# Kernel tuning notes

Measured on AMD Instinct MI355X. Metric: run time of the kernel, lower is better.

The kernel has to match this reference:

```python
import jax, jax.numpy as jnp
import numpy as np

DIM = 384
HEADS = 12
K = 3          # kernel_size
PAD = 1
STRIDE = 1
B, H, W = 8, 56, 56


def conv1x1(x, w, b=None):
    # x: [B,C,H,W], w: [O,C]
    y = jnp.einsum('bchw,oc->bohw', x, w)
    if b is not None:
        y = y + b[None, :, None, None]
    return y


def unfold(x, k, p, s):
    # torch nn.Unfold: returns patches [B, C, k*k, nH, nW], kernel row-major, channel-major overall
    Bx, C, Hx, Wx = x.shape
    nH = (Hx + 2 * p - k) // s + 1
    nW = (Wx + 2 * p - k) // s + 1
    xp = jnp.pad(x, ((0, 0), (0, 0), (p, p), (p, p)))
    cols = [xp[:, :, i:i + s * nH:s, j:j + s * nW:s] for i in range(k) for j in range(k)]
    return jnp.stack(cols, axis=2), nH, nW


def fold(col, Hx, Wx, k, p, s):
    # torch F.fold (col2im): scatter-add overlapping windows. col: [B, C, k*k, nH, nW]
    Bx, C, _, nH, nW = col.shape
    canvas = jnp.zeros((Bx, C, Hx + 2 * p, Wx + 2 * p), col.dtype)
    idx = 0
    for i in range(k):
        for j in range(k):
            canvas = canvas.at[:, :, i:i + s * nH:s, j:j + s * nW:s].add(col[:, :, idx])
            idx += 1
    return canvas[:, :, p:p + Hx, p:p + Wx]


def setup_inputs() -> dict:
    key = jax.random.key(0)
    ks = jax.random.split(key, 5)
    k2 = K * K
    x = jax.random.normal(ks[0], (B, DIM, H, W), dtype=jnp.float32)
    v_w = jax.random.normal(ks[1], (DIM, DIM), dtype=jnp.float32) * 0.02
    v_b = jnp.zeros((DIM,), dtype=jnp.float32)
    attn_w = jax.random.normal(ks[2], (k2 * k2 * HEADS, DIM), dtype=jnp.float32) * 0.02
    proj_w = jax.random.normal(ks[3], (DIM, DIM), dtype=jnp.float32) * 0.02
    return {'x': x, 'v_w': v_w, 'v_b': v_b, 'attn_w': attn_w, 'proj_w': proj_w}


def reference(x, v_w, v_b, attn_w, proj_w):
    Bx, C, Hx, Wx = x.shape
    k2 = K * K
    hd = C // HEADS  # head dim
    # value projection + unfold into overlapping k x k windows
    v = conv1x1(x, v_w, v_b)
    vcol, nH, nW = unfold(v, K, PAD, STRIDE)        # [B, C, k2, nH, nW]
    L = nH * nW
    v = vcol.reshape(Bx, HEADS, hd, k2, L)          # split C = (heads, hd), heads slow
    v = v.transpose(0, 1, 4, 3, 2)                  # [B, n, L, k2(d), hd]
    # adaptive avg pool to (nH, nW); with stride=1 this is identity (pool window 1)
    ph, pw = Hx // nH, Wx // nW
    xp = x.reshape(Bx, C, nH, ph, nW, pw).mean(axis=(3, 5))
    # per-pixel attention logits, channel layout = ((i*k2 + d)*HEADS + head)
    a = jnp.einsum('bchw,oc->bohw', xp, attn_w)     # [B, k2*k2*n, nH, nW]
    a = a.reshape(Bx, k2, k2, HEADS, L)             # [B, i, d, n, L]
    a = a.transpose(0, 3, 4, 1, 2)                  # [B, n, L, i, d]
    a = jax.nn.softmax(a, axis=-1)
    out = jnp.einsum('bnlid,bnldh->bnlih', a, v)    # [B, n, L, i, hd]
    out = out.transpose(0, 1, 4, 3, 2)              # [B, n, hd, i, L] -> channel (n*hd+h)
    out = out.reshape(Bx, C, k2, nH, nW)
    out = fold(out, Hx, Wx, K, PAD, STRIDE)         # scatter-add windows back
    return conv1x1(out, proj_w)
```

## Files before the change

kernel.cpp:

```cpp
#include <hip/hip_runtime.h>
#include <hip/hip_bf16.h>

#define DIM   384
#define HEADS 12
#define K2    9
#define HH    56
#define WW    56
#define HWP   3136
#define BB    8
#define AO    972
#define AOP   1024
#define MCAT  1408
#define PP    3200

typedef __hip_bfloat16 bf16;
typedef short bf16x8 __attribute__((ext_vector_type(8)));
typedef short bf16x4v __attribute__((ext_vector_type(4)));
typedef float f32x4 __attribute__((ext_vector_type(4)));

static __device__ __forceinline__ float b2f(bf16 v) { return __bfloat162float(v); }
static __device__ __forceinline__ float bs2f(short s) {
    return __uint_as_float(((unsigned int)(unsigned short)s) << 16);
}
static __device__ __forceinline__ float lou(unsigned int u) {
    return __uint_as_float(u << 16);
}
static __device__ __forceinline__ float hiu(unsigned int u) {
    return __uint_as_float(u & 0xffff0000u);
}
static __device__ __forceinline__ short f2bs(float f) {
    __hip_bfloat16 h = __float2bfloat16(f);
    return *(short*)&h;
}

static __device__ __forceinline__ void gl_lds16(const bf16* g, bf16* l) {
    __builtin_amdgcn_global_load_lds(
        (const __attribute__((address_space(1))) unsigned int*)g,
        (__attribute__((address_space(3))) unsigned int*)l, 16, 0, 0);
}

__global__ __launch_bounds__(256) void prep_kernel(
        const float* __restrict__ x, const float* __restrict__ v_w,
        const float* __restrict__ attn_w, const float* __restrict__ proj_w,
        bf16* __restrict__ xT, bf16* __restrict__ wcat, bf16* __restrict__ wp) {
    const int bid = blockIdx.x;
    if (bid < 400) {
        const int lane = threadIdx.x & 63, w = threadIdx.x >> 6;
        const int p = (bid % 50) * 64 + lane;
        const int b = bid / 50;
        bf16* dst = xT + ((size_t)b * PP + p) * DIM;
        if (p >= HWP) {
            bf16x8 z = {};
            for (int cg = w; cg < 48; cg += 4) *(bf16x8*)(dst + cg * 8) = z;
            return;
        }
        const float* src = x + (size_t)b * DIM * HWP + p;
        for (int cg = w; cg < 48; cg += 4) {
            bf16x8 v;
#pragma unroll
            for (int j = 0; j < 8; j++) v[j] = f2bs(src[(size_t)(cg * 8 + j) * HWP]);
            *(bf16x8*)(dst + cg * 8) = v;
        }
    } else {
        const int idx = (bid - 400) * 256 + threadIdx.x;
        const int NCAT = MCAT * DIM;
        if (idx < NCAT) {
            const int row = idx / DIM, col = idx % DIM;
            float v = 0.f;
            if (row < 384) {
                v = v_w[row * DIM + col];
            } else {
                const int q = row - 384;
                if (q < AO) {
                    const int i = q / 108, rem = q % 108;
                    const int n = rem / 9, d = rem % 9;
                    v = attn_w[((i * 9 + d) * 12 + n) * DIM + col];
                }
            }
            *(short*)&wcat[idx] = f2bs(v);
        } else {
            const int j = idx - NCAT;
            if (j < 384 * DIM) *(short*)&wp[j] = f2bs(proj_w[j]);
        }
    }
}

#define GEMM_MAIN_LOOP_V4(Ab, Bb, lA, lB, acc)                                 \
    for (int k0 = 0; k0 < DIM; k0 += 64) {                                     \
        _Pragma("unroll")                                                      \
        for (int r = 0; r < 4; r++) {                                          \
            int idx = r * 256 + t;                                             \
            int row = idx >> 3;                                                \
            int kq = ((idx & 7) - (row >> 1)) & 7;                             \
            gl_lds16(Ab + (size_t)row * DIM + k0 + kq * 8, lA + idx * 8);      \
        }                                                                      \
        _Pragma("unroll")                                                      \
        for (int r = 0; r < 4; r++) {                                          \
            int idx = r * 256 + t;                                             \
            int row = idx >> 3;                                                \
            int kq = ((idx & 7) - (row >> 1)) & 7;                             \
            gl_lds16(Bb + (size_t)row * DIM + k0 + kq * 8, lB + idx * 8);      \
        }                                                                      \
        __syncthreads();                                                       \
        _Pragma("unroll")                                                      \
        for (int h = 0; h < 2; h++) {                                          \
            const int swzh = (((h << 2) + quad + (l16 >> 1)) & 7) * 8;         \
            bf16x8 af[4], bfr[4];                                              \
            _Pragma("unroll")                                                  \
            for (int mt = 0; mt < 4; mt++)                                     \
                af[mt] = *(const bf16x8*)(lA + (wm * 64 + mt * 16 + l16) * 64 + swzh); \
            _Pragma("unroll")                                                  \
            for (int nt = 0; nt < 4; nt++)                                     \
                bfr[nt] = *(const bf16x8*)(lB + (wn * 64 + nt * 16 + l16) * 64 + swzh); \
            _Pragma("unroll")                                                  \
            for (int mt = 0; mt < 4; mt++)                                     \
                _Pragma("unroll")                                              \
                for (int nt = 0; nt < 4; nt++)                                 \
                    acc[mt][nt] = __builtin_amdgcn_mfma_f32_16x16x32_bf16(     \
                        af[mt], bfr[nt], acc[mt][nt], 0, 0, 0);                \
        }                                                                      \
        __syncthreads();                                                       \
    }

__global__ __launch_bounds__(256) void gemm12_kernel(
        const bf16* __restrict__ A, const bf16* __restrict__ Bt,
        const float* __restrict__ bias, bf16* __restrict__ vT,
        bf16* __restrict__ lT) {
    __shared__ bf16 lds[16384];
    bf16* lA = lds;
    bf16* lB = lds + 8192;
    const int t = threadIdx.x;
    const int lane = t & 63, w = t >> 6;
    const int wm = w & 1, wn = w >> 1;
    const int quad = lane >> 4, l16 = lane & 15;

    const int bid = blockIdx.x;
    const int xcd = bid & 7, slot = bid >> 3;
    const int m = slot % 11, gg = slot / 11;
    const int g = xcd + 8 * gg;
    const int n = g % 25, b = g / 25;
    const int n0 = n * 128;
    const int m0 = m * 128;

    const bf16* Ab = A + (size_t)m0 * DIM;
    const bf16* Bb = Bt + ((size_t)b * PP + n0) * DIM;

    f32x4 acc[4][4] = {};
    GEMM_MAIN_LOOP_V4(Ab, Bb, lA, lB, acc)

    const bool isv = (m0 < 384);
    bf16* outp = isv ? vT : lT;
    const int ostr = isv ? DIM : AOP;
    const int ch0 = isv ? m0 : m0 - 384;

    bf16* wbuf = lds + w * 1152;
    const int nr = lane >> 2;
    const int mc = (lane & 3) * 16;
#pragma unroll
    for (int nt = 0; nt < 4; nt++) {
#pragma unroll
        for (int mt = 0; mt < 4; mt++) {
            float4 bi = make_float4(0.f, 0.f, 0.f, 0.f);
            if (isv) bi = *(const float4*)(bias + ch0 + wm * 64 + mt * 16 + quad * 4);
            bf16x4v pk;
            pk[0] = f2bs(acc[mt][nt][0] + bi.x);
            pk[1] = f2bs(acc[mt][nt][1] + bi.y);
            pk[2] = f2bs(acc[mt][nt][2] + bi.z);
            pk[3] = f2bs(acc[mt][nt][3] + bi.w);
            *(bf16x4v*)(wbuf + l16 * 72 + mt * 16 + quad * 4) = pk;
        }
        bf16x8 v0 = *(const bf16x8*)(wbuf + nr * 72 + mc);
        bf16x8 v1 = *(const bf16x8*)(wbuf + nr * 72 + mc + 8);
        const int p = n0 + wn * 64 + nt * 16 + nr;
        if (p < HWP) {
            bf16* dp = outp + ((size_t)b * PP + p) * ostr + ch0 + wm * 64 + mc;
            *(bf16x8*)dp = v0;
            *(bf16x8*)(dp + 8) = v1;
        }
    }
}

__global__ __launch_bounds__(256) void gemm_planar_kernel(
        const bf16* __restrict__ A, const bf16* __restrict__ Bt,
        float* __restrict__ out) {
    __shared__ bf16 lds[16384];
    bf16* lA = lds;
    bf16* lB = lds + 8192;
    const int t = threadIdx.x;
    const int lane = t & 63, w = t >> 6;
    const int wm = w & 1, wn = w >> 1;
    const int quad = lane >> 4, l16 = lane & 15;

    const int bid = blockIdx.x;
    const int xcd = bid & 7, slot = bid >> 3;
    const int m = slot % 3, gg = slot / 3;
    const int g = xcd + 8 * gg;
    const int n = g % 25, b = g / 25;
    const int n0 = n * 128;
    const int m0 = m * 128;

    const bf16* Ab = A + (size_t)m0 * DIM;
    const bf16* Bb = Bt + ((size_t)b * PP + n0) * DIM;

    f32x4 acc[4][4] = {};
    GEMM_MAIN_LOOP_V4(Ab, Bb, lA, lB, acc)

#pragma unroll
    for (int mt = 0; mt < 4; mt++) {
#pragma unroll
        for (int nt = 0; nt < 4; nt++) {
            int p = n0 + wn * 64 + nt * 16 + l16;
            if (p >= HWP) continue;
#pragma unroll
            for (int reg = 0; reg < 4; reg++) {
                int o = m0 + wm * 64 + mt * 16 + quad * 4 + reg;
                out[((size_t)b * DIM + o) * HWP + p] = acc[mt][nt][reg];
            }
        }
    }
}

__global__ __launch_bounds__(384) void attn_fold_kernel(
        const bf16* __restrict__ lT, const bf16* __restrict__ vT,
        bf16* __restrict__ cT) {
    __shared__ bf16 P[8 * 9 * 12 * 9];
    __shared__ float Wf[8 * 25 * 12];
    const int t = threadIdx.x;
    const int b = blockIdx.y;
    const int pix0 = blockIdx.x * 8;
    const int Y = pix0 / WW, X0 = pix0 % WW;

    for (int r = t; r < 864; r += 384) {
        const int px = r / 108, rem = r % 108;
        const int i = rem / 12, n = rem % 12;
        const int ir = i / 3, ic = i % 3;
        const int yi = Y + 1 - ir, xi = X0 + px + 1 - ic;
        bf16* Pd = &P[r * 9];
        if (yi < 0 || yi >= HH || xi < 0 || xi >= WW) {
#pragma unroll
            for (int d = 0; d < K2; d++) *(short*)&Pd[d] = 0;
        } else {
            const bf16* rowp = lT + ((size_t)b * PP + yi * WW + xi) * AOP;
            const int e0 = i * 108 + n * 9;
            const unsigned int* up = (const unsigned int*)(rowp + (e0 & ~1));
            float el[12];
#pragma unroll
            for (int j = 0; j < 6; j++) {
                const unsigned int u = up[j];
                el[2 * j] = lou(u);
                el[2 * j + 1] = hiu(u);
            }
            const bool odd = (e0 & 1);
            float lv[K2];
#pragma unroll
            for (int d = 0; d < K2; d++) lv[d] = odd ? el[d + 1] : el[d];
            float m = -1e30f;
#pragma unroll
            for (int d = 0; d < K2; d++) m = fmaxf(m, lv[d]);
            float s = 0.f;
#pragma unroll
            for (int d = 0; d < K2; d++) { lv[d] = __expf(lv[d] - m); s += lv[d]; }
            const float inv = 1.f / s;
#pragma unroll
            for (int d = 0; d < K2; d++) *(short*)&Pd[d] = f2bs(lv[d] * inv);
        }
    }
    __syncthreads();

    for (int e = t; e < 2400; e += 384) {
        const int px = e / 300, rem = e % 300;
        const int off = rem / 12, n = rem % 12;
        const int dy = off / 5 - 2, dx = off % 5 - 2;
        const int ir_lo = max(0, -dy), ir_hi = min(2, 2 - dy);
        const int ic_lo = max(0, -dx), ic_hi = min(2, 2 - dx);
        float wsum = 0.f;
        for (int ir = ir_lo; ir <= ir_hi; ir++)
            for (int ic = ic_lo; ic <= ic_hi; ic++) {
                const int i = ir * 3 + ic;
                const int d = (dy + ir) * 3 + (dx + ic);
                wsum += b2f(P[((px * 9 + i) * 12 + n) * 9 + d]);
            }
        Wf[e] = wsum;
    }
    __syncthreads();

    const int px = t / 48, cg = t % 48;
    const int X = X0 + px;
    const int n = cg >> 2;
    const float* Wp = &Wf[px * 300];
    const bf16* vb = vT + (size_t)b * PP * DIM;
    float acc[8] = {};
#pragma unroll
    for (int dy = -2; dy <= 2; dy++) {
        const int ny = Y + dy;
        if (ny < 0 || ny >= HH) continue;
#pragma unroll
        for (int dx = -2; dx <= 2; dx++) {
            const int nx = X + dx;
            const bool ok = (nx >= 0 && nx < WW);
            const int nxc = min(max(nx, 0), WW - 1);
            const float w = ok ? Wp[((dy + 2) * 5 + dx + 2) * 12 + n] : 0.f;
            bf16x8 vv = *(const bf16x8*)(vb + (size_t)(ny * WW + nxc) * DIM + cg * 8);
#pragma unroll
            for (int j = 0; j < 8; j++) acc[j] += w * bs2f(vv[j]);
        }
    }
    bf16x8 po;
#pragma unroll
    for (int j = 0; j < 8; j++) po[j] = f2bs(acc[j]);
    *(bf16x8*)(cT + ((size_t)b * PP + pix0 + px) * DIM + cg * 8) = po;
}

extern "C" void kernel_launch(void* const* d_in, const int* in_sizes, int n_in,
                              void* d_out, int out_size, void* d_ws, size_t ws_size,
                              hipStream_t stream) {
    const float* x      = (const float*)d_in[0];
    const float* v_w    = (const float*)d_in[1];
    const float* v_b    = (const float*)d_in[2];
    const float* attn_w = (const float*)d_in[3];
    const float* proj_w = (const float*)d_in[4];
    float* out = (float*)d_out;

    bf16* xT    = (bf16*)d_ws;
    bf16* vT    = xT + (size_t)BB * PP * DIM;
    bf16* lT    = vT + (size_t)BB * PP * DIM;
    bf16* wcat  = lT + (size_t)BB * PP * AOP;
    bf16* wp    = wcat + (size_t)MCAT * DIM;
    bf16* cT    = xT;

    const int NW = MCAT * DIM + 384 * DIM;
    const int nprep = 400 + (NW + 255) / 256;
    prep_kernel<<<nprep, 256, 0, stream>>>(x, v_w, attn_w, proj_w, xT, wcat, wp);

    gemm12_kernel<<<8 * 11 * 25, 256, 0, stream>>>(wcat, xT, v_b, vT, lT);
    attn_fold_kernel<<<dim3(HWP / 8, BB), 384, 0, stream>>>(lT, vT, cT);
    gemm_planar_kernel<<<8 * 3 * 25, 256, 0, stream>>>(wp, cT, out);
}
```

Measured before the change: 223.8 us.

## Fuse softmax into logit GEMM epilogue with padded per-head layout

```diff
diff --git a/kernel.cpp b/kernel.cpp
--- a/kernel.cpp
+++ b/kernel.cpp
@@ -9,8 +9,8 @@
 #define HWP   3136
 #define BB    8
 #define AO    972
-#define AOP   1024
-#define MCAT  1408
+#define AOP   1152
+#define MCAT  1536
 #define PP    3200
 
 typedef __hip_bfloat16 bf16;
@@ -31,6 +31,10 @@
 static __device__ __forceinline__ short f2bs(float f) {
     __hip_bfloat16 h = __float2bfloat16(f);
     return *(short*)&h;
+}
+static __device__ __forceinline__ unsigned int pk2(float lo, float hi) {
+    return ((unsigned int)(unsigned short)f2bs(lo)) |
+           (((unsigned int)(unsigned short)f2bs(hi)) << 16);
 }
 
 static __device__ __forceinline__ void gl_lds16(const bf16* g, bf16* l) {
@@ -45,9 +49,12 @@
         bf16* __restrict__ xT, bf16* __restrict__ wcat, bf16* __restrict__ wp) {
     const int bid = blockIdx.x;
     if (bid < 400) {
+        const int xcd = bid & 7, slot = bid >> 3;
+        const int h = slot & 1, gg = slot >> 1;
+        const int g = xcd + 8 * gg;
+        const int n_t = g % 25, b = g / 25;
         const int lane = threadIdx.x & 63, w = threadIdx.x >> 6;
-        const int p = (bid % 50) * 64 + lane;
-        const int b = bid / 50;
+        const int p = (n_t * 2 + h) * 64 + lane;
         bf16* dst = xT + ((size_t)b * PP + p) * DIM;
         if (p >= HWP) {
             bf16x8 z = {};
@@ -71,10 +78,10 @@
                 v = v_w[row * DIM + col];
             } else {
                 const int q = row - 384;
-                if (q < AO) {
-                    const int i = q / 108, rem = q % 108;
-                    const int n = rem / 9, d = rem % 9;
-                    v = attn_w[((i * 9 + d) * 12 + n) * DIM + col];
+                const int i = q >> 7, rem = q & 127;
+                if (rem < 120) {
+                    const int n = rem / 10, d = rem % 10;
+                    if (d < 9) v = attn_w[((i * 9 + d) * 12 + n) * DIM + col];
                 }
             }
             *(short*)&wcat[idx] = f2bs(v);
@@ -136,7 +143,7 @@
 
     const int bid = blockIdx.x;
     const int xcd = bid & 7, slot = bid >> 3;
-    const int m = slot % 11, gg = slot / 11;
+    const int m = slot % 12, gg = slot / 12;
     const int g = xcd + 8 * gg;
     const int n = g % 25, b = g / 25;
     const int n0 = n * 128;
@@ -148,34 +155,84 @@
     f32x4 acc[4][4] = {};
     GEMM_MAIN_LOOP_V4(Ab, Bb, lA, lB, acc)
 
-    const bool isv = (m0 < 384);
-    bf16* outp = isv ? vT : lT;
-    const int ostr = isv ? DIM : AOP;
-    const int ch0 = isv ? m0 : m0 - 384;
-
-    bf16* wbuf = lds + w * 1152;
     const int nr = lane >> 2;
     const int mc = (lane & 3) * 16;
-#pragma unroll
-    for (int nt = 0; nt < 4; nt++) {
-#pragma unroll
-        for (int mt = 0; mt < 4; mt++) {
-            float4 bi = make_float4(0.f, 0.f, 0.f, 0.f);
-            if (isv) bi = *(const float4*)(bias + ch0 + wm * 64 + mt * 16 + quad * 4);
-            bf16x4v pk;
-            pk[0] = f2bs(acc[mt][nt][0] + bi.x);
-            pk[1] = f2bs(acc[mt][nt][1] + bi.y);
-            pk[2] = f2bs(acc[mt][nt][2] + bi.z);
-            pk[3] = f2bs(acc[mt][nt][3] + bi.w);
-            *(bf16x4v*)(wbuf + l16 * 72 + mt * 16 + quad * 4) = pk;
-        }
-        bf16x8 v0 = *(const bf16x8*)(wbuf + nr * 72 + mc);
-        bf16x8 v1 = *(const bf16x8*)(wbuf + nr * 72 + mc + 8);
-        const int p = n0 + wn * 64 + nt * 16 + nr;
-        if (p < HWP) {
-            bf16* dp = outp + ((size_t)b * PP + p) * ostr + ch0 + wm * 64 + mc;
-            *(bf16x8*)dp = v0;
-            *(bf16x8*)(dp + 8) = v1;
+
+    if (m0 < 384) {
+        bf16* wbuf = lds + w * 1152;
+#pragma unroll
+        for (int nt = 0; nt < 4; nt++) {
+#pragma unroll
+            for (int mt = 0; mt < 4; mt++) {
+                float4 bi = *(const float4*)(bias + m0 + wm * 64 + mt * 16 + quad * 4);
+                bf16x4v pk;
+                pk[0] = f2bs(acc[mt][nt][0] + bi.x);
+                pk[1] = f2bs(acc[mt][nt][1] + bi.y);
+                pk[2] = f2bs(acc[mt][nt][2] + bi.z);
+                pk[3] = f2bs(acc[mt][nt][3] + bi.w);
+                *(bf16x4v*)(wbuf + l16 * 72 + mt * 16 + quad * 4) = pk;
+            }
+            bf16x8 v0 = *(const bf16x8*)(wbuf + nr * 72 + mc);
+            bf16x8 v1 = *(const bf16x8*)(wbuf + nr * 72 + mc + 8);
+            const int p = n0 + wn * 64 + nt * 16 + nr;
+            if (p < HWP) {
+                bf16* dp = vT + ((size_t)b * PP + p) * DIM + m0 + wm * 64 + mc;
+                *(bf16x8*)dp = v0;
+                *(bf16x8*)(dp + 8) = v1;
+            }
+        }
+    } else {
+        const int i = (m0 - 384) >> 7;
+        bf16* sbuf = lds + wn * 2176;
+        const int tg = wm * 64 + lane;
+#pragma unroll
+        for (int nt = 0; nt < 4; nt++) {
+#pragma unroll
+            for (int mt = 0; mt < 4; mt++) {
+                bf16x4v pk;
+                pk[0] = f2bs(acc[mt][nt][0]);
+                pk[1] = f2bs(acc[mt][nt][1]);
+                pk[2] = f2bs(acc[mt][nt][2]);
+                pk[3] = f2bs(acc[mt][nt][3]);
+                *(bf16x4v*)(sbuf + l16 * 136 + wm * 64 + mt * 16 + quad * 4) = pk;
+            }
+            __syncthreads();
+            for (int task = tg; task < 192; task += 128) {
+                const int px = task & 15, hn = task >> 4;
+                unsigned int* row = (unsigned int*)(sbuf + px * 136 + hn * 10);
+                const unsigned int u0 = row[0], u1 = row[1], u2 = row[2],
+                                   u3 = row[3], u4 = row[4];
+                float lv[9];
+                lv[0] = lou(u0); lv[1] = hiu(u0);
+                lv[2] = lou(u1); lv[3] = hiu(u1);
+                lv[4] = lou(u2); lv[5] = hiu(u2);
+                lv[6] = lou(u3); lv[7] = hiu(u3);
+                lv[8] = lou(u4);
+                float mx = -1e30f;
+#pragma unroll
+                for (int d = 0; d < 9; d++) mx = fmaxf(mx, lv[d]);
+                float s = 0.f;
+#pragma unroll
+                for (int d = 0; d < 9; d++) { lv[d] = __expf(lv[d] - mx); s += lv[d]; }
+                const float inv = 1.f / s;
+#pragma unroll
+                for (int d = 0; d < 9; d++) lv[d] *= inv;
+                row[0] = pk2(lv[0], lv[1]);
+                row[1] = pk2(lv[2], lv[3]);
+                row[2] = pk2(lv[4], lv[5]);
+                row[3] = pk2(lv[6], lv[7]);
+                row[4] = pk2(lv[8], 0.f);
+            }
+            __syncthreads();
+            bf16x8 v0 = *(const bf16x8*)(sbuf + nr * 136 + wm * 64 + mc);
+            bf16x8 v1 = *(const bf16x8*)(sbuf + nr * 136 + wm * 64 + mc + 8);
+            const int p = n0 + wn * 64 + nt * 16 + nr;
+            if (p < HWP) {
+                bf16* dp = lT + ((size_t)b * PP + p) * AOP + i * 128 + wm * 64 + mc;
+                *(bf16x8*)dp = v0;
+                *(bf16x8*)(dp + 8) = v1;
+            }
+            __syncthreads();
         }
     }
 }
@@ -223,11 +280,18 @@
 __global__ __launch_bounds__(384) void attn_fold_kernel(
         const bf16* __restrict__ lT, const bf16* __restrict__ vT,
         bf16* __restrict__ cT) {
-    __shared__ bf16 P[8 * 9 * 12 * 9];
+    __shared__ bf16 P[8 * 9 * 12 * 10];
     __shared__ float Wf[8 * 25 * 12];
     const int t = threadIdx.x;
-    const int b = blockIdx.y;
-    const int pix0 = blockIdx.x * 8;
+
+    const int bid = blockIdx.x;
+    const int xcd = bid & 7, r0 = bid >> 3;
+    const int seg16 = r0 & 15, gg = r0 >> 4;
+    const int g = xcd + 8 * gg;
+    const int n_t = g % 25, b = g / 25;
+    const int s = n_t * 16 + seg16;
+    if (s >= HWP / 8) return;
+    const int pix0 = s * 8;
     const int Y = pix0 / WW, X0 = pix0 % WW;
 
     for (int r = t; r < 864; r += 384) {
@@ -235,34 +299,15 @@
         const int i = rem / 12, n = rem % 12;
         const int ir = i / 3, ic = i % 3;
         const int yi = Y + 1 - ir, xi = X0 + px + 1 - ic;
-        bf16* Pd = &P[r * 9];
+        unsigned int* Pd = (unsigned int*)&P[(((px * 9 + i) * 12 + n)) * 10];
         if (yi < 0 || yi >= HH || xi < 0 || xi >= WW) {
 #pragma unroll
-            for (int d = 0; d < K2; d++) *(short*)&Pd[d] = 0;
+            for (int j = 0; j < 5; j++) Pd[j] = 0;
         } else {
-            const bf16* rowp = lT + ((size_t)b * PP + yi * WW + xi) * AOP;
-            const int e0 = i * 108 + n * 9;
-            const unsigned int* up = (const unsigned int*)(rowp + (e0 & ~1));
-            float el[12];
-#pragma unroll
-            for (int j = 0; j < 6; j++) {
-                const unsigned int u = up[j];
-                el[2 * j] = lou(u);
-                el[2 * j + 1] = hiu(u);
-            }
-            const bool odd = (e0 & 1);
-            float lv[K2];
-#pragma unroll
-            for (int d = 0; d < K2; d++) lv[d] = odd ? el[d + 1] : el[d];
-            float m = -1e30f;
-#pragma unroll
-            for (int d = 0; d < K2; d++) m = fmaxf(m, lv[d]);
-            float s = 0.f;
-#pragma unroll
-            for (int d = 0; d < K2; d++) { lv[d] = __expf(lv[d] - m); s += lv[d]; }
-            const float inv = 1.f / s;
-#pragma unroll
-            for (int d = 0; d < K2; d++) *(short*)&Pd[d] = f2bs(lv[d] * inv);
+            const unsigned int* up = (const unsigned int*)
+                (lT + ((size_t)b * PP + yi * WW + xi) * AOP + i * 128 + n * 10);
+#pragma unroll
+            for (int j = 0; j < 5; j++) Pd[j] = up[j];
         }
     }
     __syncthreads();
@@ -278,7 +323,7 @@
             for (int ic = ic_lo; ic <= ic_hi; ic++) {
                 const int i = ir * 3 + ic;
                 const int d = (dy + ir) * 3 + (dx + ic);
-                wsum += b2f(P[((px * 9 + i) * 12 + n) * 9 + d]);
+                wsum += b2f(P[((px * 9 + i) * 12 + n) * 10 + d]);
             }
         Wf[e] = wsum;
     }
@@ -332,7 +377,7 @@
     const int nprep = 400 + (NW + 255) / 256;
     prep_kernel<<<nprep, 256, 0, stream>>>(x, v_w, attn_w, proj_w, xT, wcat, wp);
 
-    gemm12_kernel<<<8 * 11 * 25, 256, 0, stream>>>(wcat, xT, v_b, vT, lT);
-    attn_fold_kernel<<<dim3(HWP / 8, BB), 384, 0, stream>>>(lT, vT, cT);
+    gemm12_kernel<<<8 * 12 * 25, 256, 0, stream>>>(wcat, xT, v_b, vT, lT);
+    attn_fold_kernel<<<8 * 16 * 25, 384, 0, stream>>>(lT, vT, cT);
     gemm_planar_kernel<<<8 * 3 * 25, 256, 0, stream>>>(wp, cT, out);
 }
```

Result: no change. 225.2 us (+0.7%).
